# Kernel optimization log

Hardware: AMD Instinct MI355X
Metric: run time of the kernel (lower is better)

Reference implementation:

```python
import jax, jax.numpy as jnp
import numpy as np

B, T, TA = 16, 512, 1024
D_REG, D_AUD, HID, HEADS = 512, 512, 256, 4
NREG = 4  # mouth, left_eye, right_eye, nose (dict order)
N = NREG * B * T + B * TA  # total graph nodes


def _build_edges():
    # Faithful, vectorized version of build_graph's edge construction (phoneme_times=None).
    bs = np.arange(B)[:, None]
    ts = np.arange(T)[None, :]
    src, dst = [], []
    # cross-region same-timestep edges, all ordered pairs i != j (edge_attr 0)
    for i in range(NREG):
        for j in range(NREG):
            if i != j:
                n1 = i * B * T + bs * T + ts
                n2 = j * B * T + bs * T + ts
                src.append(n1.ravel()); dst.append(n2.ravel())
    # temporal edges within each region (edge_attr 1)
    tt = np.arange(T - 1)[None, :]
    for i in range(NREG):
        n1 = i * B * T + bs * T + tt
        src.append(n1.ravel()); dst.append((n1 + 1).ravel())
    # eye (region idx 1,2) -> audio alignment edges (edge_attr 3)
    t_aud = (np.arange(T)[None, :] * TA) // T
    audio_start = NREG * B * T
    for i in (1, 2):
        n_eye = i * B * T + bs * T + ts
        n_aud = audio_start + bs * TA + t_aud
        src.append(n_eye.ravel()); dst.append(np.broadcast_to(n_aud, (B, T)).ravel())
    # self loops (PyG GATConv default add_self_loops=True)
    loops = np.arange(N)
    src.append(loops); dst.append(loops)
    return np.concatenate(src).astype(np.int32), np.concatenate(dst).astype(np.int32)


def setup_inputs() -> dict:
    key = jax.random.key(0)
    ks = iter(jax.random.split(key, 48))
    def rn(shape, scale=1.0):
        return jax.random.normal(next(ks), shape, dtype=jnp.float32) * jnp.float32(scale)
    src_np, dst_np = _build_edges()
    inp = {
        'mouth': rn((B, T, D_REG)), 'left_eye': rn((B, T, D_REG)),
        'right_eye': rn((B, T, D_REG)), 'nose': rn((B, T, D_REG)),
        'audio_embeddings': rn((B, TA, D_AUD)),
    }
    s = 1.0 / np.sqrt(D_REG)
    for name in ['mouth', 'left_eye', 'right_eye', 'nose']:
        inp['w_' + name] = rn((D_REG, HID), s)
        inp['b_' + name] = jnp.zeros((HID,), jnp.float32)
    inp['w_audio'] = rn((D_AUD, HID), 1.0 / np.sqrt(D_AUD))
    inp['b_audio'] = jnp.zeros((HID,), jnp.float32)
    # GAT layers: layer 0 in=HID, layers 1,2 in=HID*HEADS; layers 0,1 concat, layer 2 averages heads
    dims_in = [HID, HID * HEADS, HID * HEADS]
    for l, din in enumerate(dims_in):
        concat = l < 2
        inp[f'W{l}'] = rn((din, HEADS * HID), 1.0 / np.sqrt(din))
        inp[f'as{l}'] = rn((HEADS, HID), 0.1)
        inp[f'ad{l}'] = rn((HEADS, HID), 0.1)
        inp[f'bias{l}'] = jnp.zeros((HEADS * HID,) if concat else (HID,), jnp.float32)
    inp['ln_g'] = jnp.ones((HID,), jnp.float32)
    inp['ln_b'] = jnp.zeros((HID,), jnp.float32)
    inp['src'] = jnp.asarray(src_np)
    inp['dst'] = jnp.asarray(dst_np)
    return inp


def _gat(x, W, a_s, a_d, bias, src, dst, concat):
    # PyG GATConv (eval mode): gather -> per-head attention softmax over dst -> scatter-add
    H, C = a_s.shape
    h = (x @ W).reshape(-1, H, C)                      # [N,H,C]
    alpha_s = jnp.sum(h * a_s, -1)                     # [N,H]
    alpha_d = jnp.sum(h * a_d, -1)                     # [N,H]
    e = jax.nn.leaky_relu(alpha_s[src] + alpha_d[dst], 0.2)  # [E,H]
    m = jax.ops.segment_max(e, dst, num_segments=N)
    ex = jnp.exp(e - m[dst])
    denom = jax.ops.segment_sum(ex, dst, num_segments=N)
    alpha = ex / (denom[dst] + jnp.float32(1e-16))
    out = jax.ops.segment_sum(h[src] * alpha[:, :, None], dst, num_segments=N)  # [N,H,C]
    out = out.reshape(-1, H * C) if concat else out.mean(1)
    return out + bias


def _forward(mouth, left_eye, right_eye, nose, audio_embeddings,
             w_mouth, b_mouth, w_left_eye, b_left_eye, w_right_eye, b_right_eye,
             w_nose, b_nose, w_audio, b_audio,
             W0, as0, ad0, bias0, W1, as1, ad1, bias1, W2, as2, ad2, bias2,
             ln_g, ln_b, src, dst):
    x = jnp.concatenate([
        (mouth @ w_mouth + b_mouth).reshape(B * T, HID),
        (left_eye @ w_left_eye + b_left_eye).reshape(B * T, HID),
        (right_eye @ w_right_eye + b_right_eye).reshape(B * T, HID),
        (nose @ w_nose + b_nose).reshape(B * T, HID),
        (audio_embeddings @ w_audio + b_audio).reshape(B * TA, HID),
    ], axis=0)                                          # [N,HID]
    x = _gat(x, W0, as0, ad0, bias0, src, dst, True)    # [N,HID*HEADS]
    x = _gat(x, W1, as1, ad1, bias1, src, dst, True)    # [N,HID*HEADS]
    x = _gat(x, W2, as2, ad2, bias2, src, dst, False)   # [N,HID]
    mu = x.mean(-1, keepdims=True)
    var = jnp.mean(jnp.square(x - mu), -1, keepdims=True)
    x = (x - mu) / jnp.sqrt(var + jnp.float32(1e-5)) * ln_g + ln_b
    nodes_pb = NREG * T + TA
    return x.reshape(B, nodes_pb, HID).mean(1)          # [B,HID]


def reference(mouth, left_eye, right_eye, nose, audio_embeddings,
              w_mouth, b_mouth, w_left_eye, b_left_eye, w_right_eye, b_right_eye,
              w_nose, b_nose, w_audio, b_audio,
              W0, as0, ad0, bias0, W1, as1, ad1, bias1, W2, as2, ad2, bias2,
              ln_g, ln_b, src, dst):
    return _forward(mouth, left_eye, right_eye, nose, audio_embeddings,
                    w_mouth, b_mouth, w_left_eye, b_left_eye, w_right_eye, b_right_eye,
                    w_nose, b_nose, w_audio, b_audio,
                    W0, as0, ad0, bias0, W1, as1, ad1, bias1, W2, as2, ad2, bias2,
                    ln_g, ln_b, src, dst)
```

## Files before the change

kernel.cpp:

```cpp
#include <hip/hip_runtime.h>


typedef unsigned short u16;
typedef unsigned int u32;
typedef __bf16 bf16x8 __attribute__((ext_vector_type(8)));
typedef float f32x4 __attribute__((ext_vector_type(4)));

#define ASYNC16(gp, lp)                                                        \
  __builtin_amdgcn_global_load_lds(                                            \
      (const __attribute__((address_space(1))) void*)(gp),                     \
      (__attribute__((address_space(3))) void*)(lp), 16, 0, 0)

__device__ __forceinline__ u16 f2bf(float f) {
  union { float f; u32 u; } v; v.f = f;
  u32 u = v.u + 0x7FFFu + ((v.u >> 16) & 1u);
  return (u16)(u >> 16);
}
__device__ __forceinline__ float bf2f(u16 x) {
  union { u32 u; float f; } v; v.u = ((u32)x) << 16;
  return v.f;
}
__device__ __forceinline__ float4 load_bf4(const u16* p) {
  ushort4 s = *(const ushort4*)p;
  float4 r; r.x = bf2f(s.x); r.y = bf2f(s.y); r.z = bf2f(s.z); r.w = bf2f(s.w);
  return r;
}
__device__ __forceinline__ float lrelu(float v) { return v > 0.f ? v : 0.2f * v; }
__device__ __forceinline__ float dot4(float4 a, float4 b) {
  return a.x * b.x + a.y * b.y + a.z * b.z + a.w * b.w;
}
__device__ __forceinline__ float wred(float v) {
#pragma unroll
  for (int off = 32; off; off >>= 1) v += __shfl_down(v, off);
  return v;
}
__device__ __forceinline__ float wredx(float v) {
#pragma unroll
  for (int off = 32; off; off >>= 1) v += __shfl_xor(v, off);
  return v;
}

struct PK { const float* W[8]; u16* P[8]; int KB[8]; int NN[8]; int st[9]; };
__global__ __launch_bounds__(256) void pack_kernel(PK p) {
  const int f = blockIdx.x * 4 + (threadIdx.x >> 6);
  const int lane = threadIdx.x & 63;
  int e = 0;
  while (f >= p.st[e + 1]) ++e;
  const int local = f - p.st[e];
  const int KB = p.KB[e], N = p.NN[e];
  const int nt = local / KB, kb = local % KB;
  const float* W = p.W[e] + (size_t)(kb * 32 + (lane >> 4) * 8) * N + nt * 16 + (lane & 15);
  u16* dst = p.P[e] + ((size_t)local * 64 + lane) * 8;
  u16 o[8];
#pragma unroll
  for (int j = 0; j < 8; ++j) o[j] = f2bf(W[(size_t)j * N]);
  *(uint4*)dst = *(uint4*)o;
}

__global__ __launch_bounds__(256) void gemm_kernel(
    const u16* __restrict__ A, const u16* __restrict__ Bp, u16* __restrict__ C,
    int K, int ldc) {
  __shared__ __align__(16) u16 As[2][2][128 * 32];
  const int KB = K >> 5;
  const int KB2 = K >> 6;
  const int w = blockIdx.y * 8 + blockIdx.x;
  const int xcd = w & 7, m = w >> 3;
  const int blockCol = (m & 7) * 128;
  const int blockRow = ((m >> 3) * 8 + xcd) * 128;
  const int tid = threadIdx.x;
  const int wave = tid >> 6, lane = tid & 63;
  const int wr = (wave >> 1) * 64, wc = (wave & 1) * 64;
  const int lr = lane & 15, lq = lane >> 4;
  const int sRow = wave * 16 + (lane >> 2);
  const int sGc = (lane & 3) ^ ((sRow >> 1) & 3);
  const size_t aOff0 = (size_t)(blockRow + sRow) * K + sGc * 8;
  const size_t aOff1 = aOff0 + (size_t)64 * K;
  const int ldsOff0 = wave * 512;
  const int ldsOff1 = 2048 + wave * 512;

  const u16* Bn[4];
#pragma unroll
  for (int ni = 0; ni < 4; ++ni)
    Bn[ni] = Bp + ((size_t)(((blockCol + wc) >> 4) + ni) * KB) * 512 + lane * 8;

  f32x4 acc[4][4] = {};

#pragma unroll
  for (int h = 0; h < 2; ++h) {
    ASYNC16(A + aOff0 + h * 32, As[0][h] + ldsOff0);
    ASYNC16(A + aOff1 + h * 32, As[0][h] + ldsOff1);
  }
  __syncthreads();

  for (int kb2 = 0; kb2 < KB2; ++kb2) {
    const int cb = kb2 & 1;
    if (kb2 + 1 < KB2) {
      const size_t k1 = (size_t)(kb2 + 1) * 64;
#pragma unroll
      for (int h = 0; h < 2; ++h) {
        ASYNC16(A + aOff0 + k1 + h * 32, As[cb ^ 1][h] + ldsOff0);
        ASYNC16(A + aOff1 + k1 + h * 32, As[cb ^ 1][h] + ldsOff1);
      }
    }
#pragma unroll
    for (int h = 0; h < 2; ++h) {
      const int kb = kb2 * 2 + h;
      const u16* cur = As[cb][h];
      bf16x8 bfr[4];
#pragma unroll
      for (int ni = 0; ni < 4; ++ni)
        bfr[ni] = *(const bf16x8*)(Bn[ni] + (size_t)kb * 512);
      bf16x8 af[4];
#pragma unroll
      for (int mi = 0; mi < 4; ++mi) {
        const int R = wr + mi * 16 + lr;
        const int cp = lq ^ ((R >> 1) & 3);
        af[mi] = *(const bf16x8*)(cur + R * 32 + cp * 8);
      }
#pragma unroll
      for (int mi = 0; mi < 4; ++mi)
#pragma unroll
        for (int ni = 0; ni < 4; ++ni)
          acc[mi][ni] = __builtin_amdgcn_mfma_f32_16x16x32_bf16(af[mi], bfr[ni],
                                                                acc[mi][ni], 0, 0, 0);
    }
    __syncthreads();
  }
#pragma unroll
  for (int mi = 0; mi < 4; ++mi)
#pragma unroll
    for (int ni = 0; ni < 4; ++ni) {
      const int col = blockCol + wc + ni * 16 + lr;
#pragma unroll
      for (int r = 0; r < 4; ++r) {
        const int row = blockRow + wr + mi * 16 + lq * 4 + r;
        C[(size_t)row * ldc + col] = f2bf(acc[mi][ni][r]);
      }
    }
}

struct ProjArgs { const float* x[5]; const u16* w[5]; const float* b[5]; };
__global__ __launch_bounds__(256) void proj_kernel(ProjArgs pa,
                                                   u16* __restrict__ C) {
  __shared__ __align__(16) u16 As[128 * 32];
  const int blockRow = blockIdx.y * 128, blockCol = blockIdx.x * 128;
  const int reg = blockRow >= 32768 ? 4 : (blockRow >> 13);
  const int regBase = reg == 4 ? 32768 : reg * 8192;
  const float* Af = pa.x[reg] + (size_t)(blockRow - regBase) * 512;
  const u16* Bp = pa.w[reg];
  const int tid = threadIdx.x;
  const int wave = tid >> 6, lane = tid & 63;
  const int wr = (wave >> 1) * 64, wc = (wave & 1) * 64;
  const int lr = lane & 15, lq = lane >> 4;
  const int rr = tid >> 2;
  const int cphys = tid & 3;
  const int sGc = cphys ^ ((tid >> 3) & 3);

  const u16* Bn[4];
#pragma unroll
  for (int ni = 0; ni < 4; ++ni)
    Bn[ni] = Bp + ((size_t)(((blockCol + wc) >> 4) + ni) * 16) * 512 + lane * 8;

  f32x4 acc[4][4] = {};

  for (int k0 = 0; k0 < 512; k0 += 32) {
    __syncthreads();
    bf16x8 bfr[4];
#pragma unroll
    for (int ni = 0; ni < 4; ++ni)
      bfr[ni] = *(const bf16x8*)(Bn[ni] + (size_t)k0 * 16);
#pragma unroll
    for (int i = 0; i < 2; ++i) {
      const int row = i * 64 + rr;
      const float* ap = Af + (size_t)row * 512 + k0 + sGc * 8;
      float4 f0 = *(const float4*)(ap);
      float4 f1 = *(const float4*)(ap + 4);
      uint4 pk;
      pk.x = (u32)f2bf(f0.x) | ((u32)f2bf(f0.y) << 16);
      pk.y = (u32)f2bf(f0.z) | ((u32)f2bf(f0.w) << 16);
      pk.z = (u32)f2bf(f1.x) | ((u32)f2bf(f1.y) << 16);
      pk.w = (u32)f2bf(f1.z) | ((u32)f2bf(f1.w) << 16);
      *(uint4*)(&As[row * 32 + cphys * 8]) = pk;
    }
    __syncthreads();
    bf16x8 af[4];
#pragma unroll
    for (int mi = 0; mi < 4; ++mi) {
      const int R = wr + mi * 16 + lr;
      const int cp = lq ^ ((R >> 1) & 3);
      af[mi] = *(const bf16x8*)(&As[R * 32 + cp * 8]);
    }
#pragma unroll
    for (int mi = 0; mi < 4; ++mi)
#pragma unroll
      for (int ni = 0; ni < 4; ++ni)
        acc[mi][ni] = __builtin_amdgcn_mfma_f32_16x16x32_bf16(af[mi], bfr[ni],
                                                              acc[mi][ni], 0, 0, 0);
  }
  const float* bias = pa.b[reg];
#pragma unroll
  for (int mi = 0; mi < 4; ++mi)
#pragma unroll
    for (int ni = 0; ni < 4; ++ni) {
      const int col = blockCol + wc + ni * 16 + lr;
      const float bv = bias[col];
#pragma unroll
      for (int r = 0; r < 4; ++r) {
        const int row = blockRow + wr + mi * 16 + lq * 4 + r;
        C[(size_t)row * 256 + col] = f2bf(acc[mi][ni][r] + bv);
      }
    }
}

template <bool MEAN>
__global__ __launch_bounds__(256) void agg_kernel(
    const u16* __restrict__ h, const float* __restrict__ a_s,
    const float* __restrict__ a_d, const float* __restrict__ bias,
    void* __restrict__ out) {
  const int tid = threadIdx.x;
  const int head = tid >> 6, lane = tid & 63;
  const int c4 = tid * 4;
  const float4 sa = *(const float4*)(a_s + c4);
  const float4 da = *(const float4*)(a_d + c4);
  __shared__ float asL[4][4], adL[4][4], apL[4][4];
  __shared__ float alpha[4][4][5];

  if (blockIdx.x < 8192) {
    const int bt = blockIdx.x;
    const int t = bt & 511;
    const bool hasPrev = t > 0;
    float4 hv[4], hp[4];
#pragma unroll
    for (int r = 0; r < 4; ++r)
      hv[r] = load_bf4(h + (size_t)(r * 8192 + bt) * 1024 + c4);
    if (hasPrev) {
#pragma unroll
      for (int r = 0; r < 4; ++r)
        hp[r] = load_bf4(h + (size_t)(r * 8192 + bt - 1) * 1024 + c4);
    }
#pragma unroll
    for (int r = 0; r < 4; ++r) {
      float ss = wred(dot4(hv[r], sa));
      float dd = wred(dot4(hv[r], da));
      float sp = hasPrev ? wred(dot4(hp[r], sa)) : 0.f;
      if (lane == 0) { asL[r][head] = ss; adL[r][head] = dd; apL[r][head] = sp; }
    }
    __syncthreads();
    if (tid < 16) {
      const int j = tid >> 2, hh = tid & 3;
      const float ad = adL[j][hh];
      float e[5];
#pragma unroll
      for (int r = 0; r < 4; ++r) e[r] = lrelu(asL[r][hh] + ad);
      int cnt = 4;
      if (hasPrev) { e[4] = lrelu(apL[j][hh] + ad); cnt = 5; }
      float mx = e[0];
      for (int k = 1; k < cnt; ++k) mx = fmaxf(mx, e[k]);
      float s = 0.f, ex[5];
      for (int k = 0; k < cnt; ++k) { ex[k] = __expf(e[k] - mx); s += ex[k]; }
      const float inv = 1.f / (s + 1e-16f);
#pragma unroll
      for (int k = 0; k < 5; ++k) alpha[j][hh][k] = (k < cnt) ? ex[k] * inv : 0.f;
    }
    __syncthreads();
    if constexpr (!MEAN) {
      const float4 bv = *(const float4*)(bias + c4);
      u16* ob = (u16*)out;
#pragma unroll
      for (int j = 0; j < 4; ++j) {
        const float* al = &alpha[j][head][0];
        float4 acc;
        acc.x = al[0] * hv[0].x + al[1] * hv[1].x + al[2] * hv[2].x + al[3] * hv[3].x;
        acc.y = al[0] * hv[0].y + al[1] * hv[1].y + al[2] * hv[2].y + al[3] * hv[3].y;
        acc.z = al[0] * hv[0].z + al[1] * hv[1].z + al[2] * hv[2].z + al[3] * hv[3].z;
        acc.w = al[0] * hv[0].w + al[1] * hv[1].w + al[2] * hv[2].w + al[3] * hv[3].w;
        if (hasPrev) {
          const float a4 = al[4];
          acc.x += a4 * hp[j].x; acc.y += a4 * hp[j].y;
          acc.z += a4 * hp[j].z; acc.w += a4 * hp[j].w;
        }
        ushort4 o;
        o.x = f2bf(acc.x + bv.x); o.y = f2bf(acc.y + bv.y);
        o.z = f2bf(acc.z + bv.z); o.w = f2bf(acc.w + bv.w);
        *(ushort4*)(ob + (size_t)(j * 8192 + bt) * 1024 + c4) = o;
      }
    } else {
      __shared__ float red[4][1024];
#pragma unroll
      for (int j = 0; j < 4; ++j) {
        const float* al = &alpha[j][head][0];
        float4 acc;
        acc.x = al[0] * hv[0].x + al[1] * hv[1].x + al[2] * hv[2].x + al[3] * hv[3].x;
        acc.y = al[0] * hv[0].y + al[1] * hv[1].y + al[2] * hv[2].y + al[3] * hv[3].y;
        acc.z = al[0] * hv[0].z + al[1] * hv[1].z + al[2] * hv[2].z + al[3] * hv[3].z;
        acc.w = al[0] * hv[0].w + al[1] * hv[1].w + al[2] * hv[2].w + al[3] * hv[3].w;
        if (hasPrev) {
          const float a4 = al[4];
          acc.x += a4 * hp[j].x; acc.y += a4 * hp[j].y;
          acc.z += a4 * hp[j].z; acc.w += a4 * hp[j].w;
        }
        *(float4*)(&red[j][c4]) = acc;
      }
      __syncthreads();
      const float bb = bias[tid];
      float* of = (float*)out;
#pragma unroll
      for (int j = 0; j < 4; ++j)
        of[(size_t)(j * 8192 + bt) * 256 + tid] =
            0.25f * (red[j][tid] + red[j][tid + 256] + red[j][tid + 512] +
                     red[j][tid + 768]) + bb;
    }
  } else {
    const int idx = blockIdx.x - 8192;
    const int ta = idx & 1023;
    const int node = 32768 + idx;
    const bool even = ((ta & 1) == 0);
    float4 v = load_bf4(h + (size_t)node * 1024 + c4);
    if (even) {
      const int b = idx >> 10;
      const int tt = ta >> 1;
      const int le = 8192 + b * 512 + tt;
      const int re = 16384 + b * 512 + tt;
      float4 v1 = load_bf4(h + (size_t)le * 1024 + c4);
      float4 v2 = load_bf4(h + (size_t)re * 1024 + c4);
      float s0 = wred(dot4(v, sa));
      float s1 = wred(dot4(v1, sa));
      float s2 = wred(dot4(v2, sa));
      float d0 = wred(dot4(v, da));
      if (lane == 0) {
        asL[0][head] = s0; asL[1][head] = s1; asL[2][head] = s2; adL[0][head] = d0;
      }
      __syncthreads();
      if (tid < 4) {
        const float ad = adL[0][tid];
        float e0 = lrelu(asL[0][tid] + ad);
        float e1 = lrelu(asL[1][tid] + ad);
        float e2 = lrelu(asL[2][tid] + ad);
        float mx = fmaxf(e0, fmaxf(e1, e2));
        float x0 = __expf(e0 - mx), x1 = __expf(e1 - mx), x2 = __expf(e2 - mx);
        float inv = 1.f / (x0 + x1 + x2 + 1e-16f);
        alpha[0][tid][0] = x0 * inv; alpha[0][tid][1] = x1 * inv;
        alpha[0][tid][2] = x2 * inv;
      }
      __syncthreads();
      const float a0 = alpha[0][head][0], a1 = alpha[0][head][1], a2 = alpha[0][head][2];
      v.x = a0 * v.x + a1 * v1.x + a2 * v2.x;
      v.y = a0 * v.y + a1 * v1.y + a2 * v2.y;
      v.z = a0 * v.z + a1 * v1.z + a2 * v2.z;
      v.w = a0 * v.w + a1 * v1.w + a2 * v2.w;
    }
    if constexpr (!MEAN) {
      const float4 bv = *(const float4*)(bias + c4);
      ushort4 o;
      o.x = f2bf(v.x + bv.x); o.y = f2bf(v.y + bv.y);
      o.z = f2bf(v.z + bv.z); o.w = f2bf(v.w + bv.w);
      *(ushort4*)((u16*)out + (size_t)node * 1024 + c4) = o;
    } else {
      __shared__ float redA[1024];
      *(float4*)(&redA[c4]) = v;
      __syncthreads();
      float* of = (float*)out;
      of[(size_t)node * 256 + tid] =
          0.25f * (redA[tid] + redA[tid + 256] + redA[tid + 512] + redA[tid + 768]) +
          bias[tid];
    }
  }
}

__global__ __launch_bounds__(256) void ln_pool_kernel(
    const float* __restrict__ xf, const float* __restrict__ g,
    const float* __restrict__ bb, float* __restrict__ part) {
  const int tid = threadIdx.x;
  const int wave = tid >> 6, lane = tid & 63;
  const int node0 = blockIdx.x * 64 + wave * 16;
  const float4 g4 = *(const float4*)(g + lane * 4);
  const float4 b4 = *(const float4*)(bb + lane * 4);
  float4 acc = {0.f, 0.f, 0.f, 0.f};
  for (int i = 0; i < 16; ++i) {
    const float4 v = *(const float4*)(xf + (size_t)(node0 + i) * 256 + lane * 4);
    const float s = wredx(v.x + v.y + v.z + v.w);
    const float q = wredx(v.x * v.x + v.y * v.y + v.z * v.z + v.w * v.w);
    const float mean = s * (1.f / 256.f);
    const float var = q * (1.f / 256.f) - mean * mean;
    const float rstd = rsqrtf(var + 1e-5f);
    acc.x += (v.x - mean) * rstd * g4.x + b4.x;
    acc.y += (v.y - mean) * rstd * g4.y + b4.y;
    acc.z += (v.z - mean) * rstd * g4.z + b4.z;
    acc.w += (v.w - mean) * rstd * g4.w + b4.w;
  }
  *(float4*)(part + (size_t)(blockIdx.x * 4 + wave) * 256 + lane * 4) = acc;
}

__global__ __launch_bounds__(256) void pool2_kernel(const float* __restrict__ part,
                                                    float* __restrict__ out) {
  const int chunk = blockIdx.x;
  const int c = threadIdx.x;
  float s = 0.f;
  for (int i = 0; i < 192; ++i) s += part[(size_t)(chunk * 192 + i) * 256 + c];
  out[chunk * 256 + c] = s * (1.f / 3072.f);
}

extern "C" void kernel_launch(void* const* d_in, const int* in_sizes, int n_in,
                              void* d_out, int out_size, void* d_ws, size_t ws_size,
                              hipStream_t stream) {
  const float* x_reg[4] = {(const float*)d_in[0], (const float*)d_in[1],
                           (const float*)d_in[2], (const float*)d_in[3]};
  const float* audio = (const float*)d_in[4];
  const float* w_reg[4] = {(const float*)d_in[5], (const float*)d_in[7],
                           (const float*)d_in[9], (const float*)d_in[11]};
  const float* b_reg[4] = {(const float*)d_in[6], (const float*)d_in[8],
                           (const float*)d_in[10], (const float*)d_in[12]};
  const float* w_aud = (const float*)d_in[13];
  const float* b_aud = (const float*)d_in[14];
  const float* Wl[3] = {(const float*)d_in[15], (const float*)d_in[19],
                        (const float*)d_in[23]};
  const float* as_in[3] = {(const float*)d_in[16], (const float*)d_in[20],
                           (const float*)d_in[24]};
  const float* ad_in[3] = {(const float*)d_in[17], (const float*)d_in[21],
                           (const float*)d_in[25]};
  const float* bias_l[3] = {(const float*)d_in[18], (const float*)d_in[22],
                            (const float*)d_in[26]};
  const float* ln_g = (const float*)d_in[27];
  const float* ln_b = (const float*)d_in[28];

  char* ws = (char*)d_ws;
  u16* h_bf = (u16*)ws;
  float* part = (float*)ws;
  u16* xb = (u16*)(ws + 100663296);
  float* xf = (float*)xb;
  u16* wt = (u16*)(ws + 201326592);

  u16* wtp[5];
  for (int r = 0; r < 5; ++r) wtp[r] = wt + (size_t)r * 131072;
  u16* wt0 = wt + 655360;
  u16* wt1 = wt + 917504;
  u16* wt2 = wt + 1966080;

  PK pk;
  for (int r = 0; r < 4; ++r) { pk.W[r] = w_reg[r]; pk.P[r] = wtp[r]; pk.KB[r] = 16; pk.NN[r] = 256; }
  pk.W[4] = w_aud; pk.P[4] = wtp[4]; pk.KB[4] = 16; pk.NN[4] = 256;
  pk.W[5] = Wl[0]; pk.P[5] = wt0; pk.KB[5] = 8;  pk.NN[5] = 1024;
  pk.W[6] = Wl[1]; pk.P[6] = wt1; pk.KB[6] = 32; pk.NN[6] = 1024;
  pk.W[7] = Wl[2]; pk.P[7] = wt2; pk.KB[7] = 32; pk.NN[7] = 1024;
  pk.st[0] = 0;
  {
    const int nfr[8] = {256, 256, 256, 256, 256, 512, 2048, 2048};
    int acc = 0;
    for (int e = 0; e < 8; ++e) { acc += nfr[e]; pk.st[e + 1] = acc; }
  }
  pack_kernel<<<pk.st[8] / 4, 256, 0, stream>>>(pk);

  ProjArgs pa;
  for (int r = 0; r < 4; ++r) { pa.x[r] = x_reg[r]; pa.w[r] = wtp[r]; pa.b[r] = b_reg[r]; }
  pa.x[4] = audio; pa.w[4] = wtp[4]; pa.b[4] = b_aud;
  proj_kernel<<<dim3(2, 384), 256, 0, stream>>>(pa, xb);

  const u16* wl[3] = {wt0, wt1, wt2};
  const int Kl[3] = {256, 1024, 1024};
  for (int l = 0; l < 3; ++l) {
    gemm_kernel<<<dim3(8, 384), 256, 0, stream>>>(xb, wl[l], h_bf, Kl[l], 1024);
    if (l < 2)
      agg_kernel<false><<<24576, 256, 0, stream>>>(h_bf, as_in[l], ad_in[l],
                                                   bias_l[l], xb);
    else
      agg_kernel<true><<<24576, 256, 0, stream>>>(h_bf, as_in[l], ad_in[l],
                                                  bias_l[l], xf);
  }

  ln_pool_kernel<<<768, 256, 0, stream>>>(xf, ln_g, ln_b, part);
  pool2_kernel<<<16, 256, 0, stream>>>(part, (float*)d_out);
}
```

Before: 637.7 us.

## Fuse LayerNorm and mean pooling into final GAT aggregation with time-chunked blocks

The aggregation kernel now gives each block 8 consecutive timesteps, so each previous-timestep row is reused from registers instead of reloaded, and each audio block handles two nodes. The last layer's aggregation also applies LayerNorm and accumulates per-batch pooled sums with atomics, which removes the fp32 node-feature write/read and the separate ln_pool/pool2 kernels. Small zero and scale kernels are added. The cost is fewer blocks (9216 vs 24576), serial per-timestep syncs inside a block, and nondeterministic float atomic summation order.

```diff
diff --git a/kernel.cpp b/kernel.cpp
--- a/kernel.cpp
+++ b/kernel.cpp
@@ -216,56 +216,62 @@
 __global__ __launch_bounds__(256) void agg_kernel(
     const u16* __restrict__ h, const float* __restrict__ a_s,
     const float* __restrict__ a_d, const float* __restrict__ bias,
+    const float* __restrict__ lng, const float* __restrict__ lnb,
     void* __restrict__ out) {
   const int tid = threadIdx.x;
   const int head = tid >> 6, lane = tid & 63;
   const int c4 = tid * 4;
   const float4 sa = *(const float4*)(a_s + c4);
   const float4 da = *(const float4*)(a_d + c4);
-  __shared__ float asL[4][4], adL[4][4], apL[4][4];
-  __shared__ float alpha[4][4][5];
-
-  if (blockIdx.x < 8192) {
-    const int bt = blockIdx.x;
-    const int t = bt & 511;
-    const bool hasPrev = t > 0;
-    float4 hv[4], hp[4];
-#pragma unroll
-    for (int r = 0; r < 4; ++r)
-      hv[r] = load_bf4(h + (size_t)(r * 8192 + bt) * 1024 + c4);
-    if (hasPrev) {
-#pragma unroll
-      for (int r = 0; r < 4; ++r)
-        hp[r] = load_bf4(h + (size_t)(r * 8192 + bt - 1) * 1024 + c4);
-    }
-#pragma unroll
-    for (int r = 0; r < 4; ++r) {
-      float ss = wred(dot4(hv[r], sa));
-      float dd = wred(dot4(hv[r], da));
-      float sp = hasPrev ? wred(dot4(hp[r], sa)) : 0.f;
-      if (lane == 0) { asL[r][head] = ss; adL[r][head] = dd; apL[r][head] = sp; }
-    }
-    __syncthreads();
-    if (tid < 16) {
-      const int j = tid >> 2, hh = tid & 3;
-      const float ad = adL[j][hh];
-      float e[5];
-#pragma unroll
-      for (int r = 0; r < 4; ++r) e[r] = lrelu(asL[r][hh] + ad);
-      int cnt = 4;
-      if (hasPrev) { e[4] = lrelu(apL[j][hh] + ad); cnt = 5; }
-      float mx = e[0];
-      for (int k = 1; k < cnt; ++k) mx = fmaxf(mx, e[k]);
-      float s = 0.f, ex[5];
-      for (int k = 0; k < cnt; ++k) { ex[k] = __expf(e[k] - mx); s += ex[k]; }
-      const float inv = 1.f / (s + 1e-16f);
-#pragma unroll
-      for (int k = 0; k < 5; ++k) alpha[j][hh][k] = (k < cnt) ? ex[k] * inv : 0.f;
-    }
-    __syncthreads();
-    if constexpr (!MEAN) {
-      const float4 bv = *(const float4*)(bias + c4);
-      u16* ob = (u16*)out;
+  __shared__ float asB[2][4][4], adL[4][4], alpha[4][4][5];
+  __shared__ float red[MEAN ? 4096 : 1];
+  __shared__ float ls[MEAN ? 32 : 1];
+
+  if (blockIdx.x < 1024) {
+    const int b = blockIdx.x >> 6;
+    const int t0 = (blockIdx.x & 63) * 8;
+    float4 hprev[4] = {};
+    if (t0 > 0) {
+      const int btp = b * 512 + t0 - 1;
+#pragma unroll
+      for (int r = 0; r < 4; ++r) {
+        hprev[r] = load_bf4(h + (size_t)(r * 8192 + btp) * 1024 + c4);
+        float sp = wred(dot4(hprev[r], sa));
+        if (lane == 0) asB[1][r][head] = sp;
+      }
+    }
+    __syncthreads();
+    float pacc[4] = {};
+    int pch[4] = {-1, -1, -1, -1};
+    for (int tt = 0; tt < 8; ++tt) {
+      const int t = t0 + tt, bt = b * 512 + t;
+      const bool hasPrev = (t > 0);
+      float4 hv[4];
+#pragma unroll
+      for (int r = 0; r < 4; ++r) {
+        hv[r] = load_bf4(h + (size_t)(r * 8192 + bt) * 1024 + c4);
+        float ss = wred(dot4(hv[r], sa));
+        float dd = wred(dot4(hv[r], da));
+        if (lane == 0) { asB[tt & 1][r][head] = ss; adL[r][head] = dd; }
+      }
+      __syncthreads();
+      if (tid < 16) {
+        const int j = tid >> 2, hh = tid & 3;
+        const float ad = adL[j][hh];
+        float e[5];
+#pragma unroll
+        for (int r = 0; r < 4; ++r) e[r] = lrelu(asB[tt & 1][r][hh] + ad);
+        int cnt = 4;
+        if (hasPrev) { e[4] = lrelu(asB[(tt & 1) ^ 1][j][hh] + ad); cnt = 5; }
+        float mx = e[0];
+        for (int k = 1; k < cnt; ++k) mx = fmaxf(mx, e[k]);
+        float s = 0.f, ex[5];
+        for (int k = 0; k < cnt; ++k) { ex[k] = __expf(e[k] - mx); s += ex[k]; }
+        const float inv = 1.f / (s + 1e-16f);
+#pragma unroll
+        for (int k = 0; k < 5; ++k) alpha[j][hh][k] = (k < cnt) ? ex[k] * inv : 0.f;
+      }
+      __syncthreads();
 #pragma unroll
       for (int j = 0; j < 4; ++j) {
         const float* al = &alpha[j][head][0];
@@ -276,128 +282,147 @@
         acc.w = al[0] * hv[0].w + al[1] * hv[1].w + al[2] * hv[2].w + al[3] * hv[3].w;
         if (hasPrev) {
           const float a4 = al[4];
-          acc.x += a4 * hp[j].x; acc.y += a4 * hp[j].y;
-          acc.z += a4 * hp[j].z; acc.w += a4 * hp[j].w;
+          acc.x += a4 * hprev[j].x; acc.y += a4 * hprev[j].y;
+          acc.z += a4 * hprev[j].z; acc.w += a4 * hprev[j].w;
         }
-        ushort4 o;
-        o.x = f2bf(acc.x + bv.x); o.y = f2bf(acc.y + bv.y);
-        o.z = f2bf(acc.z + bv.z); o.w = f2bf(acc.w + bv.w);
-        *(ushort4*)(ob + (size_t)(j * 8192 + bt) * 1024 + c4) = o;
-      }
+        if constexpr (!MEAN) {
+          const float4 bv = *(const float4*)(bias + c4);
+          ushort4 o;
+          o.x = f2bf(acc.x + bv.x); o.y = f2bf(acc.y + bv.y);
+          o.z = f2bf(acc.z + bv.z); o.w = f2bf(acc.w + bv.w);
+          *(ushort4*)((u16*)out + (size_t)(j * 8192 + bt) * 1024 + c4) = o;
+        } else {
+          *(float4*)(&red[j * 1024 + c4]) = acc;
+        }
+      }
+      if constexpr (MEAN) {
+        __syncthreads();
+        const float bb = bias[tid];
+        float v[4];
+#pragma unroll
+        for (int j = 0; j < 4; ++j) {
+          v[j] = 0.25f * (red[j * 1024 + tid] + red[j * 1024 + tid + 256] +
+                          red[j * 1024 + tid + 512] + red[j * 1024 + tid + 768]) + bb;
+          const float sj = wredx(v[j]);
+          const float qj = wredx(v[j] * v[j]);
+          if (lane == 0) { ls[head * 8 + j * 2] = sj; ls[head * 8 + j * 2 + 1] = qj; }
+        }
+        __syncthreads();
+#pragma unroll
+        for (int j = 0; j < 4; ++j) {
+          const float S = ls[j * 2] + ls[8 + j * 2] + ls[16 + j * 2] + ls[24 + j * 2];
+          const float Q = ls[j * 2 + 1] + ls[8 + j * 2 + 1] + ls[16 + j * 2 + 1] +
+                          ls[24 + j * 2 + 1];
+          const float mean = S * (1.f / 256.f);
+          const float var = Q * (1.f / 256.f) - mean * mean;
+          const float n = (v[j] - mean) * rsqrtf(var + 1e-5f) * lng[tid] + lnb[tid];
+          const int ch = (j * 8192 + bt) / 3072;
+          if (ch != pch[j]) {
+            if (pch[j] >= 0) atomicAdd((float*)out + pch[j] * 256 + tid, pacc[j]);
+            pacc[j] = 0.f; pch[j] = ch;
+          }
+          pacc[j] += n;
+        }
+      }
+#pragma unroll
+      for (int r = 0; r < 4; ++r) hprev[r] = hv[r];
+    }
+    if constexpr (MEAN) {
+#pragma unroll
+      for (int j = 0; j < 4; ++j)
+        if (pch[j] >= 0) atomicAdd((float*)out + pch[j] * 256 + tid, pacc[j]);
+    }
+  } else {
+    const int aid = blockIdx.x - 1024;
+    const int idx0 = aid * 2;
+    const int b = idx0 >> 10;
+    const int ta0 = idx0 & 1023;
+    const int n0 = 32768 + idx0, n1 = n0 + 1;
+    const int tt2 = ta0 >> 1;
+    const int le = 8192 + b * 512 + tt2;
+    const int re = 16384 + b * 512 + tt2;
+    float4 v0 = load_bf4(h + (size_t)n0 * 1024 + c4);
+    float4 vo = load_bf4(h + (size_t)n1 * 1024 + c4);
+    float4 v1 = load_bf4(h + (size_t)le * 1024 + c4);
+    float4 v2 = load_bf4(h + (size_t)re * 1024 + c4);
+    {
+      float s0 = wred(dot4(v0, sa));
+      float s1 = wred(dot4(v1, sa));
+      float s2 = wred(dot4(v2, sa));
+      float d0 = wred(dot4(v0, da));
+      if (lane == 0) {
+        asB[0][0][head] = s0; asB[0][1][head] = s1; asB[0][2][head] = s2;
+        adL[0][head] = d0;
+      }
+    }
+    __syncthreads();
+    if (tid < 4) {
+      const float ad = adL[0][tid];
+      float e0 = lrelu(asB[0][0][tid] + ad);
+      float e1 = lrelu(asB[0][1][tid] + ad);
+      float e2 = lrelu(asB[0][2][tid] + ad);
+      float mx = fmaxf(e0, fmaxf(e1, e2));
+      float x0 = __expf(e0 - mx), x1 = __expf(e1 - mx), x2 = __expf(e2 - mx);
+      float inv = 1.f / (x0 + x1 + x2 + 1e-16f);
+      alpha[0][tid][0] = x0 * inv; alpha[0][tid][1] = x1 * inv;
+      alpha[0][tid][2] = x2 * inv;
+    }
+    __syncthreads();
+    const float a0 = alpha[0][head][0], a1 = alpha[0][head][1], a2 = alpha[0][head][2];
+    v0.x = a0 * v0.x + a1 * v1.x + a2 * v2.x;
+    v0.y = a0 * v0.y + a1 * v1.y + a2 * v2.y;
+    v0.z = a0 * v0.z + a1 * v1.z + a2 * v2.z;
+    v0.w = a0 * v0.w + a1 * v1.w + a2 * v2.w;
+    if constexpr (!MEAN) {
+      const float4 bv = *(const float4*)(bias + c4);
+      ushort4 oe, oo;
+      oe.x = f2bf(v0.x + bv.x); oe.y = f2bf(v0.y + bv.y);
+      oe.z = f2bf(v0.z + bv.z); oe.w = f2bf(v0.w + bv.w);
+      oo.x = f2bf(vo.x + bv.x); oo.y = f2bf(vo.y + bv.y);
+      oo.z = f2bf(vo.z + bv.z); oo.w = f2bf(vo.w + bv.w);
+      *(ushort4*)((u16*)out + (size_t)n0 * 1024 + c4) = oe;
+      *(ushort4*)((u16*)out + (size_t)n1 * 1024 + c4) = oo;
     } else {
-      __shared__ float red[4][1024];
-#pragma unroll
-      for (int j = 0; j < 4; ++j) {
-        const float* al = &alpha[j][head][0];
-        float4 acc;
-        acc.x = al[0] * hv[0].x + al[1] * hv[1].x + al[2] * hv[2].x + al[3] * hv[3].x;
-        acc.y = al[0] * hv[0].y + al[1] * hv[1].y + al[2] * hv[2].y + al[3] * hv[3].y;
-        acc.z = al[0] * hv[0].z + al[1] * hv[1].z + al[2] * hv[2].z + al[3] * hv[3].z;
-        acc.w = al[0] * hv[0].w + al[1] * hv[1].w + al[2] * hv[2].w + al[3] * hv[3].w;
-        if (hasPrev) {
-          const float a4 = al[4];
-          acc.x += a4 * hp[j].x; acc.y += a4 * hp[j].y;
-          acc.z += a4 * hp[j].z; acc.w += a4 * hp[j].w;
-        }
-        *(float4*)(&red[j][c4]) = acc;
-      }
+      *(float4*)(&red[c4]) = v0;
+      *(float4*)(&red[1024 + c4]) = vo;
       __syncthreads();
       const float bb = bias[tid];
-      float* of = (float*)out;
-#pragma unroll
-      for (int j = 0; j < 4; ++j)
-        of[(size_t)(j * 8192 + bt) * 256 + tid] =
-            0.25f * (red[j][tid] + red[j][tid + 256] + red[j][tid + 512] +
-                     red[j][tid + 768]) + bb;
-    }
-  } else {
-    const int idx = blockIdx.x - 8192;
-    const int ta = idx & 1023;
-    const int node = 32768 + idx;
-    const bool even = ((ta & 1) == 0);
-    float4 v = load_bf4(h + (size_t)node * 1024 + c4);
-    if (even) {
-      const int b = idx >> 10;
-      const int tt = ta >> 1;
-      const int le = 8192 + b * 512 + tt;
-      const int re = 16384 + b * 512 + tt;
-      float4 v1 = load_bf4(h + (size_t)le * 1024 + c4);
-      float4 v2 = load_bf4(h + (size_t)re * 1024 + c4);
-      float s0 = wred(dot4(v, sa));
-      float s1 = wred(dot4(v1, sa));
-      float s2 = wred(dot4(v2, sa));
-      float d0 = wred(dot4(v, da));
+      float vA = 0.25f * (red[tid] + red[tid + 256] + red[tid + 512] + red[tid + 768]) + bb;
+      float vB = 0.25f * (red[1024 + tid] + red[1024 + tid + 256] +
+                          red[1024 + tid + 512] + red[1024 + tid + 768]) + bb;
+      const float sA = wredx(vA), qA = wredx(vA * vA);
+      const float sB = wredx(vB), qB = wredx(vB * vB);
       if (lane == 0) {
-        asL[0][head] = s0; asL[1][head] = s1; asL[2][head] = s2; adL[0][head] = d0;
+        ls[head * 8] = sA; ls[head * 8 + 1] = qA;
+        ls[head * 8 + 2] = sB; ls[head * 8 + 3] = qB;
       }
       __syncthreads();
-      if (tid < 4) {
-        const float ad = adL[0][tid];
-        float e0 = lrelu(asL[0][tid] + ad);
-        float e1 = lrelu(asL[1][tid] + ad);
-        float e2 = lrelu(asL[2][tid] + ad);
-        float mx = fmaxf(e0, fmaxf(e1, e2));
-        float x0 = __expf(e0 - mx), x1 = __expf(e1 - mx), x2 = __expf(e2 - mx);
-        float inv = 1.f / (x0 + x1 + x2 + 1e-16f);
-        alpha[0][tid][0] = x0 * inv; alpha[0][tid][1] = x1 * inv;
-        alpha[0][tid][2] = x2 * inv;
-      }
-      __syncthreads();
-      const float a0 = alpha[0][head][0], a1 = alpha[0][head][1], a2 = alpha[0][head][2];
-      v.x = a0 * v.x + a1 * v1.x + a2 * v2.x;
-      v.y = a0 * v.y + a1 * v1.y + a2 * v2.y;
-      v.z = a0 * v.z + a1 * v1.z + a2 * v2.z;
-      v.w = a0 * v.w + a1 * v1.w + a2 * v2.w;
-    }
-    if constexpr (!MEAN) {
-      const float4 bv = *(const float4*)(bias + c4);
-      ushort4 o;
-      o.x = f2bf(v.x + bv.x); o.y = f2bf(v.y + bv.y);
-      o.z = f2bf(v.z + bv.z); o.w = f2bf(v.w + bv.w);
-      *(ushort4*)((u16*)out + (size_t)node * 1024 + c4) = o;
-    } else {
-      __shared__ float redA[1024];
-      *(float4*)(&redA[c4]) = v;
-      __syncthreads();
-      float* of = (float*)out;
-      of[(size_t)node * 256 + tid] =
-          0.25f * (redA[tid] + redA[tid + 256] + redA[tid + 512] + redA[tid + 768]) +
-          bias[tid];
-    }
-  }
-}
-
-__global__ __launch_bounds__(256) void ln_pool_kernel(
-    const float* __restrict__ xf, const float* __restrict__ g,
-    const float* __restrict__ bb, float* __restrict__ part) {
-  const int tid = threadIdx.x;
-  const int wave = tid >> 6, lane = tid & 63;
-  const int node0 = blockIdx.x * 64 + wave * 16;
-  const float4 g4 = *(const float4*)(g + lane * 4);
-  const float4 b4 = *(const float4*)(bb + lane * 4);
-  float4 acc = {0.f, 0.f, 0.f, 0.f};
-  for (int i = 0; i < 16; ++i) {
-    const float4 v = *(const float4*)(xf + (size_t)(node0 + i) * 256 + lane * 4);
-    const float s = wredx(v.x + v.y + v.z + v.w);
-    const float q = wredx(v.x * v.x + v.y * v.y + v.z * v.z + v.w * v.w);
-    const float mean = s * (1.f / 256.f);
-    const float var = q * (1.f / 256.f) - mean * mean;
-    const float rstd = rsqrtf(var + 1e-5f);
-    acc.x += (v.x - mean) * rstd * g4.x + b4.x;
-    acc.y += (v.y - mean) * rstd * g4.y + b4.y;
-    acc.z += (v.z - mean) * rstd * g4.z + b4.z;
-    acc.w += (v.w - mean) * rstd * g4.w + b4.w;
-  }
-  *(float4*)(part + (size_t)(blockIdx.x * 4 + wave) * 256 + lane * 4) = acc;
-}
-
-__global__ __launch_bounds__(256) void pool2_kernel(const float* __restrict__ part,
-                                                    float* __restrict__ out) {
-  const int chunk = blockIdx.x;
-  const int c = threadIdx.x;
-  float s = 0.f;
-  for (int i = 0; i < 192; ++i) s += part[(size_t)(chunk * 192 + i) * 256 + c];
-  out[chunk * 256 + c] = s * (1.f / 3072.f);
+      const float SA = ls[0] + ls[8] + ls[16] + ls[24];
+      const float QA = ls[1] + ls[9] + ls[17] + ls[25];
+      const float SB = ls[2] + ls[10] + ls[18] + ls[26];
+      const float QB = ls[3] + ls[11] + ls[19] + ls[27];
+      const float mA = SA * (1.f / 256.f), vrA = QA * (1.f / 256.f) - mA * mA;
+      const float mB = SB * (1.f / 256.f), vrB = QB * (1.f / 256.f) - mB * mB;
+      const float g = lng[tid], be = lnb[tid];
+      const float nA = (vA - mA) * rsqrtf(vrA + 1e-5f) * g + be;
+      const float nB = (vB - mB) * rsqrtf(vrB + 1e-5f) * g + be;
+      const int ch0 = n0 / 3072, ch1 = n1 / 3072;
+      if (ch0 == ch1) {
+        atomicAdd((float*)out + ch0 * 256 + tid, nA + nB);
+      } else {
+        atomicAdd((float*)out + ch0 * 256 + tid, nA);
+        atomicAdd((float*)out + ch1 * 256 + tid, nB);
+      }
+    }
+  }
+}
+
+__global__ __launch_bounds__(256) void zero_kernel(float* __restrict__ p) {
+  p[blockIdx.x * 256 + threadIdx.x] = 0.f;
+}
+__global__ __launch_bounds__(256) void scale_kernel(float* __restrict__ p) {
+  const int i = blockIdx.x * 256 + threadIdx.x;
+  p[i] *= (1.f / 3072.f);
 }
 
 extern "C" void kernel_launch(void* const* d_in, const int* in_sizes, int n_in,
@@ -425,9 +450,7 @@
 
   char* ws = (char*)d_ws;
   u16* h_bf = (u16*)ws;
-  float* part = (float*)ws;
   u16* xb = (u16*)(ws + 100663296);
-  float* xf = (float*)xb;
   u16* wt = (u16*)(ws + 201326592);
 
   u16* wtp[5];
@@ -449,6 +472,7 @@
     for (int e = 0; e < 8; ++e) { acc += nfr[e]; pk.st[e + 1] = acc; }
   }
   pack_kernel<<<pk.st[8] / 4, 256, 0, stream>>>(pk);
+  zero_kernel<<<16, 256, 0, stream>>>((float*)d_out);
 
   ProjArgs pa;
   for (int r = 0; r < 4; ++r) { pa.x[r] = x_reg[r]; pa.w[r] = wtp[r]; pa.b[r] = b_reg[r]; }
@@ -460,13 +484,12 @@
   for (int l = 0; l < 3; ++l) {
     gemm_kernel<<<dim3(8, 384), 256, 0, stream>>>(xb, wl[l], h_bf, Kl[l], 1024);
     if (l < 2)
-      agg_kernel<false><<<24576, 256, 0, stream>>>(h_bf, as_in[l], ad_in[l],
-                                                   bias_l[l], xb);
+      agg_kernel<false><<<9216, 256, 0, stream>>>(h_bf, as_in[l], ad_in[l],
+                                                  bias_l[l], nullptr, nullptr, xb);
     else
-      agg_kernel<true><<<24576, 256, 0, stream>>>(h_bf, as_in[l], ad_in[l],
-                                                  bias_l[l], xf);
-  }
-
-  ln_pool_kernel<<<768, 256, 0, stream>>>(xf, ln_g, ln_b, part);
-  pool2_kernel<<<16, 256, 0, stream>>>(part, (float*)d_out);
-}
+      agg_kernel<true><<<9216, 256, 0, stream>>>(h_bf, as_in[l], ad_in[l],
+                                                 bias_l[l], ln_g, ln_b, d_out);
+  }
+
+  scale_kernel<<<16, 256, 0, stream>>>((float*)d_out);
+}
```

Result: slower. 687.8 us (+7.9%).

## Fuse audio-node aggregation into per-timestep region blocks of GAT aggregation

Applied to the files above, without the earlier changes.

Each aggregation block now handles one (batch, timestep) and also processes the two audio nodes aligned to it, so the separate 16384 audio blocks go away. The even audio node reuses the left/right eye features and source scores the block already loaded, which avoids re-reading those rows from global memory. The launch shrinks from 24576 to 8192 blocks. In exchange each block does more work, holds more registers, and in the mean variant uses 24KB of dynamic LDS, which may lower occupancy.

```diff
diff --git a/kernel.cpp b/kernel.cpp
--- a/kernel.cpp
+++ b/kernel.cpp
@@ -217,152 +217,129 @@
     const u16* __restrict__ h, const float* __restrict__ a_s,
     const float* __restrict__ a_d, const float* __restrict__ bias,
     void* __restrict__ out) {
+  extern __shared__ float red[];
   const int tid = threadIdx.x;
   const int head = tid >> 6, lane = tid & 63;
   const int c4 = tid * 4;
   const float4 sa = *(const float4*)(a_s + c4);
   const float4 da = *(const float4*)(a_d + c4);
-  __shared__ float asL[4][4], adL[4][4], apL[4][4];
-  __shared__ float alpha[4][4][5];
-
-  if (blockIdx.x < 8192) {
-    const int bt = blockIdx.x;
-    const int t = bt & 511;
-    const bool hasPrev = t > 0;
-    float4 hv[4], hp[4];
+  __shared__ float asL[4][4], adL[4][4], apL[4][4], aeS[4], aeD[4];
+  __shared__ float alpha[4][4][5], alphaA[4][3];
+
+  const int bt = blockIdx.x;
+  const int b = bt >> 9, t = bt & 511;
+  const bool hasPrev = t > 0;
+  const int nodeE = 32768 + b * 1024 + 2 * t;
+  const int nodeO = nodeE + 1;
+
+  float4 hv[4], hp[4];
+#pragma unroll
+  for (int r = 0; r < 4; ++r)
+    hv[r] = load_bf4(h + (size_t)(r * 8192 + bt) * 1024 + c4);
+  float4 hae = load_bf4(h + (size_t)nodeE * 1024 + c4);
+  float4 hao = load_bf4(h + (size_t)nodeO * 1024 + c4);
+  if (hasPrev) {
 #pragma unroll
     for (int r = 0; r < 4; ++r)
-      hv[r] = load_bf4(h + (size_t)(r * 8192 + bt) * 1024 + c4);
+      hp[r] = load_bf4(h + (size_t)(r * 8192 + bt - 1) * 1024 + c4);
+  }
+#pragma unroll
+  for (int r = 0; r < 4; ++r) {
+    float ss = wred(dot4(hv[r], sa));
+    float dd = wred(dot4(hv[r], da));
+    float sp = hasPrev ? wred(dot4(hp[r], sa)) : 0.f;
+    if (lane == 0) { asL[r][head] = ss; adL[r][head] = dd; apL[r][head] = sp; }
+  }
+  {
+    float se = wred(dot4(hae, sa));
+    float de = wred(dot4(hae, da));
+    if (lane == 0) { aeS[head] = se; aeD[head] = de; }
+  }
+  __syncthreads();
+  if (tid < 16) {
+    const int j = tid >> 2, hh = tid & 3;
+    const float ad = adL[j][hh];
+    float e[5];
+#pragma unroll
+    for (int r = 0; r < 4; ++r) e[r] = lrelu(asL[r][hh] + ad);
+    int cnt = 4;
+    if (hasPrev) { e[4] = lrelu(apL[j][hh] + ad); cnt = 5; }
+    float mx = e[0];
+    for (int k = 1; k < cnt; ++k) mx = fmaxf(mx, e[k]);
+    float s = 0.f, ex[5];
+    for (int k = 0; k < cnt; ++k) { ex[k] = __expf(e[k] - mx); s += ex[k]; }
+    const float inv = 1.f / (s + 1e-16f);
+#pragma unroll
+    for (int k = 0; k < 5; ++k) alpha[j][hh][k] = (k < cnt) ? ex[k] * inv : 0.f;
+  } else if (tid < 20) {
+    const int hh = tid - 16;
+    const float ad = aeD[hh];
+    const float e0 = lrelu(aeS[hh] + ad);
+    const float e1 = lrelu(asL[1][hh] + ad);
+    const float e2 = lrelu(asL[2][hh] + ad);
+    const float mx = fmaxf(e0, fmaxf(e1, e2));
+    const float x0 = __expf(e0 - mx), x1 = __expf(e1 - mx), x2 = __expf(e2 - mx);
+    const float inv = 1.f / (x0 + x1 + x2 + 1e-16f);
+    alphaA[hh][0] = x0 * inv; alphaA[hh][1] = x1 * inv; alphaA[hh][2] = x2 * inv;
+  }
+  __syncthreads();
+
+  float4 av[6];
+#pragma unroll
+  for (int j = 0; j < 4; ++j) {
+    const float* al = &alpha[j][head][0];
+    float4 acc;
+    acc.x = al[0] * hv[0].x + al[1] * hv[1].x + al[2] * hv[2].x + al[3] * hv[3].x;
+    acc.y = al[0] * hv[0].y + al[1] * hv[1].y + al[2] * hv[2].y + al[3] * hv[3].y;
+    acc.z = al[0] * hv[0].z + al[1] * hv[1].z + al[2] * hv[2].z + al[3] * hv[3].z;
+    acc.w = al[0] * hv[0].w + al[1] * hv[1].w + al[2] * hv[2].w + al[3] * hv[3].w;
     if (hasPrev) {
-#pragma unroll
-      for (int r = 0; r < 4; ++r)
-        hp[r] = load_bf4(h + (size_t)(r * 8192 + bt - 1) * 1024 + c4);
-    }
-#pragma unroll
-    for (int r = 0; r < 4; ++r) {
-      float ss = wred(dot4(hv[r], sa));
-      float dd = wred(dot4(hv[r], da));
-      float sp = hasPrev ? wred(dot4(hp[r], sa)) : 0.f;
-      if (lane == 0) { asL[r][head] = ss; adL[r][head] = dd; apL[r][head] = sp; }
-    }
+      const float a4 = al[4];
+      acc.x += a4 * hp[j].x; acc.y += a4 * hp[j].y;
+      acc.z += a4 * hp[j].z; acc.w += a4 * hp[j].w;
+    }
+    av[j] = acc;
+  }
+  {
+    const float a0 = alphaA[head][0], a1 = alphaA[head][1], a2 = alphaA[head][2];
+    float4 acc;
+    acc.x = a0 * hae.x + a1 * hv[1].x + a2 * hv[2].x;
+    acc.y = a0 * hae.y + a1 * hv[1].y + a2 * hv[2].y;
+    acc.z = a0 * hae.z + a1 * hv[1].z + a2 * hv[2].z;
+    acc.w = a0 * hae.w + a1 * hv[1].w + a2 * hv[2].w;
+    av[4] = acc;
+    av[5] = hao;
+  }
+
+  if constexpr (!MEAN) {
+    const float4 bv = *(const float4*)(bias + c4);
+    u16* ob = (u16*)out;
+    size_t rows[6];
+#pragma unroll
+    for (int j = 0; j < 4; ++j) rows[j] = (size_t)(j * 8192 + bt);
+    rows[4] = (size_t)nodeE; rows[5] = (size_t)nodeO;
+#pragma unroll
+    for (int k = 0; k < 6; ++k) {
+      ushort4 o;
+      o.x = f2bf(av[k].x + bv.x); o.y = f2bf(av[k].y + bv.y);
+      o.z = f2bf(av[k].z + bv.z); o.w = f2bf(av[k].w + bv.w);
+      *(ushort4*)(ob + rows[k] * 1024 + c4) = o;
+    }
+  } else {
+#pragma unroll
+    for (int k = 0; k < 6; ++k) *(float4*)(&red[k * 1024 + c4]) = av[k];
     __syncthreads();
-    if (tid < 16) {
-      const int j = tid >> 2, hh = tid & 3;
-      const float ad = adL[j][hh];
-      float e[5];
-#pragma unroll
-      for (int r = 0; r < 4; ++r) e[r] = lrelu(asL[r][hh] + ad);
-      int cnt = 4;
-      if (hasPrev) { e[4] = lrelu(apL[j][hh] + ad); cnt = 5; }
-      float mx = e[0];
-      for (int k = 1; k < cnt; ++k) mx = fmaxf(mx, e[k]);
-      float s = 0.f, ex[5];
-      for (int k = 0; k < cnt; ++k) { ex[k] = __expf(e[k] - mx); s += ex[k]; }
-      const float inv = 1.f / (s + 1e-16f);
-#pragma unroll
-      for (int k = 0; k < 5; ++k) alpha[j][hh][k] = (k < cnt) ? ex[k] * inv : 0.f;
-    }
-    __syncthreads();
-    if constexpr (!MEAN) {
-      const float4 bv = *(const float4*)(bias + c4);
-      u16* ob = (u16*)out;
-#pragma unroll
-      for (int j = 0; j < 4; ++j) {
-        const float* al = &alpha[j][head][0];
-        float4 acc;
-        acc.x = al[0] * hv[0].x + al[1] * hv[1].x + al[2] * hv[2].x + al[3] * hv[3].x;
-        acc.y = al[0] * hv[0].y + al[1] * hv[1].y + al[2] * hv[2].y + al[3] * hv[3].y;
-        acc.z = al[0] * hv[0].z + al[1] * hv[1].z + al[2] * hv[2].z + al[3] * hv[3].z;
-        acc.w = al[0] * hv[0].w + al[1] * hv[1].w + al[2] * hv[2].w + al[3] * hv[3].w;
-        if (hasPrev) {
-          const float a4 = al[4];
-          acc.x += a4 * hp[j].x; acc.y += a4 * hp[j].y;
-          acc.z += a4 * hp[j].z; acc.w += a4 * hp[j].w;
-        }
-        ushort4 o;
-        o.x = f2bf(acc.x + bv.x); o.y = f2bf(acc.y + bv.y);
-        o.z = f2bf(acc.z + bv.z); o.w = f2bf(acc.w + bv.w);
-        *(ushort4*)(ob + (size_t)(j * 8192 + bt) * 1024 + c4) = o;
-      }
-    } else {
-      __shared__ float red[4][1024];
-#pragma unroll
-      for (int j = 0; j < 4; ++j) {
-        const float* al = &alpha[j][head][0];
-        float4 acc;
-        acc.x = al[0] * hv[0].x + al[1] * hv[1].x + al[2] * hv[2].x + al[3] * hv[3].x;
-        acc.y = al[0] * hv[0].y + al[1] * hv[1].y + al[2] * hv[2].y + al[3] * hv[3].y;
-        acc.z = al[0] * hv[0].z + al[1] * hv[1].z + al[2] * hv[2].z + al[3] * hv[3].z;
-        acc.w = al[0] * hv[0].w + al[1] * hv[1].w + al[2] * hv[2].w + al[3] * hv[3].w;
-        if (hasPrev) {
-          const float a4 = al[4];
-          acc.x += a4 * hp[j].x; acc.y += a4 * hp[j].y;
-          acc.z += a4 * hp[j].z; acc.w += a4 * hp[j].w;
-        }
-        *(float4*)(&red[j][c4]) = acc;
-      }
-      __syncthreads();
-      const float bb = bias[tid];
-      float* of = (float*)out;
-#pragma unroll
-      for (int j = 0; j < 4; ++j)
-        of[(size_t)(j * 8192 + bt) * 256 + tid] =
-            0.25f * (red[j][tid] + red[j][tid + 256] + red[j][tid + 512] +
-                     red[j][tid + 768]) + bb;
-    }
-  } else {
-    const int idx = blockIdx.x - 8192;
-    const int ta = idx & 1023;
-    const int node = 32768 + idx;
-    const bool even = ((ta & 1) == 0);
-    float4 v = load_bf4(h + (size_t)node * 1024 + c4);
-    if (even) {
-      const int b = idx >> 10;
-      const int tt = ta >> 1;
-      const int le = 8192 + b * 512 + tt;
-      const int re = 16384 + b * 512 + tt;
-      float4 v1 = load_bf4(h + (size_t)le * 1024 + c4);
-      float4 v2 = load_bf4(h + (size_t)re * 1024 + c4);
-      float s0 = wred(dot4(v, sa));
-      float s1 = wred(dot4(v1, sa));
-      float s2 = wred(dot4(v2, sa));
-      float d0 = wred(dot4(v, da));
-      if (lane == 0) {
-        asL[0][head] = s0; asL[1][head] = s1; asL[2][head] = s2; adL[0][head] = d0;
-      }
-      __syncthreads();
-      if (tid < 4) {
-        const float ad = adL[0][tid];
-        float e0 = lrelu(asL[0][tid] + ad);
-        float e1 = lrelu(asL[1][tid] + ad);
-        float e2 = lrelu(asL[2][tid] + ad);
-        float mx = fmaxf(e0, fmaxf(e1, e2));
-        float x0 = __expf(e0 - mx), x1 = __expf(e1 - mx), x2 = __expf(e2 - mx);
-        float inv = 1.f / (x0 + x1 + x2 + 1e-16f);
-        alpha[0][tid][0] = x0 * inv; alpha[0][tid][1] = x1 * inv;
-        alpha[0][tid][2] = x2 * inv;
-      }
-      __syncthreads();
-      const float a0 = alpha[0][head][0], a1 = alpha[0][head][1], a2 = alpha[0][head][2];
-      v.x = a0 * v.x + a1 * v1.x + a2 * v2.x;
-      v.y = a0 * v.y + a1 * v1.y + a2 * v2.y;
-      v.z = a0 * v.z + a1 * v1.z + a2 * v2.z;
-      v.w = a0 * v.w + a1 * v1.w + a2 * v2.w;
-    }
-    if constexpr (!MEAN) {
-      const float4 bv = *(const float4*)(bias + c4);
-      ushort4 o;
-      o.x = f2bf(v.x + bv.x); o.y = f2bf(v.y + bv.y);
-      o.z = f2bf(v.z + bv.z); o.w = f2bf(v.w + bv.w);
-      *(ushort4*)((u16*)out + (size_t)node * 1024 + c4) = o;
-    } else {
-      __shared__ float redA[1024];
-      *(float4*)(&redA[c4]) = v;
-      __syncthreads();
-      float* of = (float*)out;
-      of[(size_t)node * 256 + tid] =
-          0.25f * (redA[tid] + redA[tid + 256] + redA[tid + 512] + redA[tid + 768]) +
-          bias[tid];
+    const float bb = bias[tid];
+    float* of = (float*)out;
+    size_t rows[6];
+#pragma unroll
+    for (int j = 0; j < 4; ++j) rows[j] = (size_t)(j * 8192 + bt);
+    rows[4] = (size_t)nodeE; rows[5] = (size_t)nodeO;
+#pragma unroll
+    for (int k = 0; k < 6; ++k) {
+      const float v = 0.25f * (red[k * 1024 + tid] + red[k * 1024 + tid + 256] +
+                               red[k * 1024 + tid + 512] + red[k * 1024 + tid + 768]) + bb;
+      of[rows[k] * 256 + tid] = v;
     }
   }
 }
@@ -457,14 +434,15 @@
 
   const u16* wl[3] = {wt0, wt1, wt2};
   const int Kl[3] = {256, 1024, 1024};
+  const size_t dynLds = 6 * 1024 * sizeof(float);
   for (int l = 0; l < 3; ++l) {
     gemm_kernel<<<dim3(8, 384), 256, 0, stream>>>(xb, wl[l], h_bf, Kl[l], 1024);
     if (l < 2)
-      agg_kernel<false><<<24576, 256, 0, stream>>>(h_bf, as_in[l], ad_in[l],
-                                                   bias_l[l], xb);
+      agg_kernel<false><<<8192, 256, 0, stream>>>(h_bf, as_in[l], ad_in[l],
+                                                  bias_l[l], xb);
     else
-      agg_kernel<true><<<24576, 256, 0, stream>>>(h_bf, as_in[l], ad_in[l],
-                                                  bias_l[l], xf);
+      agg_kernel<true><<<8192, 256, dynLds, stream>>>(h_bf, as_in[l], ad_in[l],
+                                                      bias_l[l], xf);
   }
 
   ln_pool_kernel<<<768, 256, 0, stream>>>(xf, ln_g, ln_b, part);
```

After: 616.9 us. -3.3%, faster.
